# Optimization experiments

Measured on AMD Instinct MI355X. Metric: run time of the kernel, lower is better.

Reference implementation:

```python
import jax, jax.numpy as jnp
import numpy as np

B, N, FIN = 32, 1024, 6
KCHEB = 3
CLASS_NUM = 40


def _pairwise_adj(x):
    # x: [B, N, D] -> exp(-squared_euclidean_dist) adjacency [B, N, N]
    inner = jnp.einsum('bnd,bmd->bnm', x, x)
    sq = jnp.sum(x * x, axis=-1)
    d2 = sq[:, :, None] - 2.0 * inner + sq[:, None, :]
    return jnp.exp(-d2)


def _get_laplacian(adj):
    # normalized Laplacian: I - D^{-1/2} A D^{-1/2}
    deg = jnp.sum(adj, axis=-1)                       # [B, N]
    d_is = 1.0 / jnp.sqrt(deg)                        # [B, N]
    eye = jnp.eye(adj.shape[-1], dtype=adj.dtype)
    return eye - d_is[:, :, None] * adj * d_is[:, None, :]


def _cheb_conv(x, L, W, b):
    # Chebyshev graph conv: sum_k T_k(L) x W_k + b;  W: [K, Fin, Fout]
    x0 = x
    x1 = jnp.einsum('bnm,bmf->bnf', L, x0)
    out = jnp.einsum('bnf,fg->bng', x0, W[0]) + jnp.einsum('bnf,fg->bng', x1, W[1])
    xk_2, xk_1 = x0, x1
    for k in range(2, W.shape[0]):
        xk = 2.0 * jnp.einsum('bnm,bmf->bnf', L, xk_1) - xk_2
        out = out + jnp.einsum('bnf,fg->bng', xk, W[k])
        xk_2, xk_1 = xk_1, xk
    return out + b


def setup_inputs() -> dict:
    key = jax.random.key(0)
    ks = jax.random.split(key, 16)

    def w(k, shape, fan_in):
        return jax.random.normal(k, shape, dtype=jnp.float32) / np.sqrt(fan_in)

    return {
        'x': jax.random.normal(ks[0], (B, N, FIN), dtype=jnp.float32),
        'W1': w(ks[1], (KCHEB, 6, 128), 6 * KCHEB),
        'b1': jnp.zeros((128,), jnp.float32),
        'W2': w(ks[2], (KCHEB, 128, 512), 128 * KCHEB),
        'b2': jnp.zeros((512,), jnp.float32),
        'W3': w(ks[3], (KCHEB, 512, 1024), 512 * KCHEB),
        'b3': jnp.zeros((1024,), jnp.float32),
        'fc1_w': w(ks[4], (1024, 512), 1024),
        'fc1_b': jnp.zeros((512,), jnp.float32),
        'fc2_w': w(ks[5], (512, 128), 512),
        'fc2_b': jnp.zeros((128,), jnp.float32),
        'fc3_w': w(ks[6], (128, CLASS_NUM), 128),
        'fc3_b': jnp.zeros((CLASS_NUM,), jnp.float32),
    }


def reference(x, W1, b1, W2, b2, W3, b3, fc1_w, fc1_b, fc2_w, fc2_b, fc3_w, fc3_b):
    # Laplacians are computed under torch.no_grad in the original
    L = _get_laplacian(_pairwise_adj(x))
    out = jax.nn.relu(_cheb_conv(x, L, W1, b1))        # [B, N, 128]

    L = _get_laplacian(_pairwise_adj(out))
    out = jax.nn.relu(_cheb_conv(out, L, W2, b2))      # [B, N, 512]

    L = _get_laplacian(_pairwise_adj(out))
    out = jax.nn.relu(_cheb_conv(out, L, W3, b3))      # [B, N, 1024]

    out = jnp.max(out, axis=1)                          # global max pool -> [B, 1024]
    out = jax.nn.relu(out @ fc1_w + fc1_b)              # dropout is identity at eval
    out = jax.nn.relu(out @ fc2_w + fc2_b)
    out = out @ fc3_w + fc3_b                           # [B, CLASS_NUM]
    return out
```

## Files before the change

### kernel.cpp

```cpp
#include <hip/hip_runtime.h>
#include <cstddef>


#define NN 1024

typedef unsigned short ushort_t;
typedef __bf16 bf16x8 __attribute__((ext_vector_type(8)));
typedef float f32x4 __attribute__((ext_vector_type(4)));

__device__ inline ushort_t f2bf(float f) {
    unsigned int u = __float_as_uint(f);
    u = (u + 0x7fffu + ((u >> 16) & 1u)) >> 16;
    return (ushort_t)u;
}
__device__ inline float bf2f(ushort_t s) {
    return __uint_as_float(((unsigned int)s) << 16);
}

__device__ __attribute__((always_inline)) inline void gld16(
    const ushort_t* g, ushort_t* l) {
    __builtin_amdgcn_global_load_lds(
        (__attribute__((address_space(1))) void*)(ushort_t*)g,
        (__attribute__((address_space(3))) void*)l, 16, 0, 0);
}

__global__ void zero_kernel(float* __restrict__ p, int n) {
    int i = blockIdx.x * blockDim.x + threadIdx.x;
    if (i < n) p[i] = 0.f;
}

__global__ __launch_bounds__(256) void wconvT_kernel(
    const float* __restrict__ W, ushort_t* __restrict__ Wt, int Fi, int Fo, int Ks) {
    int p = blockIdx.z;
    int k0 = blockIdx.y * 64, g0 = blockIdx.x * 64;
    __shared__ float T[64][65];
    int t = threadIdx.x;
#pragma unroll
    for (int q = 0; q < 16; ++q) {
        int kr = (t >> 6) + 4 * q, gc = t & 63;
        int k = k0 + kr, g = g0 + gc;
        T[kr][gc] = (k < Fi && g < Fo) ? W[((size_t)p * Fi + k) * Fo + g] : 0.f;
    }
    __syncthreads();
#pragma unroll
    for (int q = 0; q < 16; ++q) {
        int gr = (t >> 6) + 4 * q, kc = t & 63;
        int g = g0 + gr, k = k0 + kc;
        if (g < Fo && k < Ks)
            Wt[((size_t)p * Fo + g) * Ks + k] = f2bf(T[kc][gr]);
    }
}

__global__ __launch_bounds__(256) void prep2_kernel(
    const float* __restrict__ X, ushort_t* __restrict__ hi, ushort_t* __restrict__ lo,
    ushort_t* __restrict__ Xt, float* __restrict__ sq, int F, int Fp, int bsh) {
    int L = blockIdx.x;
    int b = L & ((1 << bsh) - 1), n0 = (L >> bsh) * 64;
    int t = threadIdx.x;
    __shared__ float T[64][65];
    __shared__ float red[4][64];
    const float* Xb = X + ((size_t)b * NN + n0) * F;
    float sacc = 0.f;

    for (int f0 = 0; f0 < Fp; f0 += 64) {
        __syncthreads();
#pragma unroll
        for (int p = 0; p < 16; ++p) {
            int nr = (t >> 6) + 4 * p, fc = t & 63;
            int f = f0 + fc;
            T[nr][fc] = (f < F) ? Xb[(size_t)nr * F + f] : 0.f;
        }
        __syncthreads();
#pragma unroll
        for (int p = 0; p < 16; ++p) {
            int nr = (t >> 6) + 4 * p, fc = t & 63;
            int f = f0 + fc;
            if (f < Fp) {
                float x = T[nr][fc];
                ushort_t h = f2bf(x);
                size_t off = ((size_t)b * NN + n0 + nr) * Fp + f;
                hi[off] = h;
                lo[off] = f2bf(x - bf2f(h));
            }
        }
#pragma unroll
        for (int p = 0; p < 16; ++p) {
            int fr = (t >> 6) + 4 * p;
            int f = f0 + fr;
            if (f < F)
                Xt[((size_t)b * Fp + f) * NN + n0 + (t & 63)] = f2bf(T[t & 63][fr]);
        }
        {
            int nl = t & 63, fq = t >> 6;
#pragma unroll
            for (int fc = 0; fc < 16; ++fc) {
                float v = T[nl][fq * 16 + fc];
                sacc += v * v;
            }
        }
    }
    red[t >> 6][t & 63] = sacc;
    __syncthreads();
    if (t < 64)
        sq[(size_t)b * NN + n0 + t] = red[0][t] + red[1][t] + red[2][t] + red[3][t];
}

__global__ __launch_bounds__(256) void adj_kernel(
    const ushort_t* __restrict__ hi, const ushort_t* __restrict__ lo,
    const float* __restrict__ sq, ushort_t* __restrict__ Abf,
    float* __restrict__ deg_part, int Fp, int bsh, int BCv) {
    int t = threadIdx.x;
    int L = blockIdx.x;
    int b = L & ((1 << bsh) - 1);
    int rest = L >> bsh;
    int m0 = (rest & 7) * 128, n0 = (rest >> 3) * 128;
    const ushort_t* Hb = hi + (size_t)b * NN * Fp;
    const ushort_t* Lb = lo + (size_t)b * NN * Fp;
    ushort_t* Ab = Abf + (size_t)b * NN * NN;
    const float* sqb = sq + (size_t)b * NN;

    int lane = t & 63, quad = lane >> 4, l16 = lane & 15, wave = t >> 6;
    int rowoff = (wave >> 1) * 64, coloff = (wave & 1) * 64;

    __shared__ __align__(16) ushort_t smem[40960];

    f32x4 acc[4][4];
#pragma unroll
    for (int i = 0; i < 4; ++i)
#pragma unroll
        for (int j = 0; j < 4; ++j) acc[i][j] = (f32x4){0.f, 0.f, 0.f, 0.f};

    int rr0 = t >> 2, kq = (t & 3) * 8;
    int rr1 = rr0 + 64;
    const ushort_t* pAh0 = Hb + (size_t)(n0 + rr0) * Fp + kq;
    const ushort_t* pAh1 = Hb + (size_t)(n0 + rr1) * Fp + kq;
    const ushort_t* pAl0 = Lb + (size_t)(n0 + rr0) * Fp + kq;
    const ushort_t* pAl1 = Lb + (size_t)(n0 + rr1) * Fp + kq;
    const ushort_t* pBh0 = Hb + (size_t)(m0 + rr0) * Fp + kq;
    const ushort_t* pBh1 = Hb + (size_t)(m0 + rr1) * Fp + kq;
    const ushort_t* pBl0 = Lb + (size_t)(m0 + rr0) * Fp + kq;
    const ushort_t* pBl1 = Lb + (size_t)(m0 + rr1) * Fp + kq;
    int o0 = rr0 * 40 + kq, o1 = rr1 * 40 + kq;

    {
        *(uint4*)&smem[o0]         = *(const uint4*)pAh0;
        *(uint4*)&smem[o1]         = *(const uint4*)pAh1;
        *(uint4*)&smem[5120 + o0]  = *(const uint4*)pAl0;
        *(uint4*)&smem[5120 + o1]  = *(const uint4*)pAl1;
        *(uint4*)&smem[10240 + o0] = *(const uint4*)pBh0;
        *(uint4*)&smem[10240 + o1] = *(const uint4*)pBh1;
        *(uint4*)&smem[15360 + o0] = *(const uint4*)pBl0;
        *(uint4*)&smem[15360 + o1] = *(const uint4*)pBl1;
    }
    __syncthreads();

    int NIT = Fp >> 5;
    for (int it = 0; it < NIT; ++it) {
        int cur = (it & 1) * 20480;
        int nxt = 20480 - cur;
        uint4 rh0, rh1, rl0, rl1, sh0, sh1, sl0, sl1;
        if (it + 1 < NIT) {
            int k = (it + 1) * 32;
            rh0 = *(const uint4*)(pAh0 + k); rh1 = *(const uint4*)(pAh1 + k);
            rl0 = *(const uint4*)(pAl0 + k); rl1 = *(const uint4*)(pAl1 + k);
            sh0 = *(const uint4*)(pBh0 + k); sh1 = *(const uint4*)(pBh1 + k);
            sl0 = *(const uint4*)(pBl0 + k); sl1 = *(const uint4*)(pBl1 + k);
        }
        ushort_t* Ah = smem + cur;
        ushort_t* Al = smem + cur + 5120;
        ushort_t* Bh = smem + cur + 10240;
        ushort_t* Bl = smem + cur + 15360;
        bf16x8 ah[4], al[4], bh[4], bl[4];
#pragma unroll
        for (int i = 0; i < 4; ++i) {
            ah[i] = *(const bf16x8*)&Ah[(rowoff + i * 16 + l16) * 40 + quad * 8];
            al[i] = *(const bf16x8*)&Al[(rowoff + i * 16 + l16) * 40 + quad * 8];
        }
#pragma unroll
        for (int j = 0; j < 4; ++j) {
            bh[j] = *(const bf16x8*)&Bh[(coloff + j * 16 + l16) * 40 + quad * 8];
            bl[j] = *(const bf16x8*)&Bl[(coloff + j * 16 + l16) * 40 + quad * 8];
        }
#pragma unroll
        for (int i = 0; i < 4; ++i)
#pragma unroll
            for (int j = 0; j < 4; ++j) {
                acc[i][j] = __builtin_amdgcn_mfma_f32_16x16x32_bf16(al[i], bh[j], acc[i][j], 0, 0, 0);
                acc[i][j] = __builtin_amdgcn_mfma_f32_16x16x32_bf16(ah[i], bl[j], acc[i][j], 0, 0, 0);
                acc[i][j] = __builtin_amdgcn_mfma_f32_16x16x32_bf16(ah[i], bh[j], acc[i][j], 0, 0, 0);
            }
        if (it + 1 < NIT) {
            *(uint4*)&smem[nxt + o0]         = rh0;
            *(uint4*)&smem[nxt + o1]         = rh1;
            *(uint4*)&smem[nxt + 5120 + o0]  = rl0;
            *(uint4*)&smem[nxt + 5120 + o1]  = rl1;
            *(uint4*)&smem[nxt + 10240 + o0] = sh0;
            *(uint4*)&smem[nxt + 10240 + o1] = sh1;
            *(uint4*)&smem[nxt + 15360 + o0] = sl0;
            *(uint4*)&smem[nxt + 15360 + o1] = sl1;
        }
        __syncthreads();
    }

    float rs[4][4];
#pragma unroll
    for (int i = 0; i < 4; ++i)
#pragma unroll
        for (int r = 0; r < 4; ++r) rs[i][r] = 0.f;

#pragma unroll
    for (int j = 0; j < 4; ++j) {
        int m = m0 + coloff + j * 16 + l16;
        float sm = sqb[m];
#pragma unroll
        for (int i = 0; i < 4; ++i) {
#pragma unroll
            for (int r = 0; r < 4; ++r) {
                int n = n0 + rowoff + i * 16 + quad * 4 + r;
                float v = __expf(2.f * acc[i][j][r] - sqb[n] - sm);
                Ab[(size_t)n * NN + m] = f2bf(v);
                rs[i][r] += v;
            }
        }
    }
    int slot = (rest & 7) * 2 + (wave & 1);
#pragma unroll
    for (int i = 0; i < 4; ++i)
#pragma unroll
        for (int r = 0; r < 4; ++r) {
            float s = rs[i][r];
            s += __shfl_xor(s, 1);
            s += __shfl_xor(s, 2);
            s += __shfl_xor(s, 4);
            s += __shfl_xor(s, 8);
            if (l16 == 0)
                deg_part[((size_t)slot * BCv + b) * NN + n0 + rowoff + i * 16 + quad * 4 + r] = s;
        }
}

__global__ __launch_bounds__(256) void disscale_kernel(
    ushort_t* __restrict__ Xt, const float* __restrict__ deg_part,
    float* __restrict__ dis, int Fp, int bsh, int BCv) {
    int L = blockIdx.x;
    int b = L & ((1 << bsh) - 1), n0 = (L >> bsh) * 64;
    int t = threadIdx.x;
    __shared__ float dloc[64];
    if (t < 64) {
        float s = 0.f;
#pragma unroll
        for (int k = 0; k < 16; ++k) s += deg_part[((size_t)k * BCv + b) * NN + n0 + t];
        float d = rsqrtf(s);
        dloc[t] = d;
        dis[(size_t)b * NN + n0 + t] = d;
    }
    __syncthreads();
    int lane = t & 63, fq = t >> 6;
    float d = dloc[lane];
    ushort_t* Xb = Xt + (size_t)b * Fp * NN + n0 + lane;
    for (int f = fq; f < Fp; f += 4) {
        size_t off = (size_t)f * NN;
        Xb[off] = f2bf(bf2f(Xb[off]) * d);
    }
}

__global__ __launch_bounds__(256) void lx_kernel(
    const ushort_t* __restrict__ Abf, const float* __restrict__ dis,
    const ushort_t* __restrict__ in_t, const ushort_t* __restrict__ x0t,
    ushort_t* __restrict__ out_t, ushort_t* __restrict__ out_b,
    int F, int Fp, int mode, int ft, int bsh) {
    int t = threadIdx.x;
    int L = blockIdx.x;
    int b = L & ((1 << bsh) - 1);
    int rest = L >> bsh;
    int m0 = (rest % ft) * 128;
    int n0 = (rest / ft) * 64;
    const ushort_t* Ain = in_t + (size_t)b * Fp * NN;
    const ushort_t* Ab = Abf + (size_t)b * NN * NN;

    int lane = t & 63, quad = lane >> 4, l16 = lane & 15, wave = t >> 6;
    int rowoff = wave * 32;

    __shared__ __align__(16) ushort_t smem[18432];

    f32x4 acc[2][4];
#pragma unroll
    for (int i = 0; i < 2; ++i)
#pragma unroll
        for (int j = 0; j < 4; ++j) acc[i][j] = (f32x4){0.f, 0.f, 0.f, 0.f};

    int lr = lane >> 2, lk = (lane & 3) * 8;
    int rbase = wave * 32;
    const ushort_t* gA = Ain + (size_t)(m0 + rbase + lr) * NN + lk;
    const ushort_t* gB = Ab + (size_t)(n0 + wave * 16 + lr) * NN + lk;

#define LX_STAGE(BOFF, CI)                                            \
    {                                                                 \
        int k_ = (CI) * 32;                                           \
        ushort_t* As_ = smem + (BOFF);                                \
        gld16(gA + k_, As_ + rbase * 32);                             \
        gld16(gA + (size_t)16 * NN + k_, As_ + rbase * 32 + 512);     \
        gld16(gB + k_, As_ + 4096 + wave * 16 * 32);                  \
    }
#define LX_COMP(BOFF)                                                            \
    {                                                                            \
        ushort_t* As_ = smem + (BOFF);                                           \
        ushort_t* Bs_ = As_ + 4096;                                              \
        bf16x8 af[2], bfv[4];                                                    \
        _Pragma("unroll")                                                        \
        for (int i = 0; i < 2; ++i)                                              \
            af[i] = *(const bf16x8*)&As_[(rowoff + i * 16 + l16) * 32 + quad * 8]; \
        _Pragma("unroll")                                                        \
        for (int j = 0; j < 4; ++j)                                              \
            bfv[j] = *(const bf16x8*)&Bs_[(j * 16 + l16) * 32 + quad * 8];       \
        _Pragma("unroll")                                                        \
        for (int i = 0; i < 2; ++i)                                              \
            _Pragma("unroll")                                                    \
            for (int j = 0; j < 4; ++j)                                          \
                acc[i][j] = __builtin_amdgcn_mfma_f32_16x16x32_bf16(af[i], bfv[j], acc[i][j], 0, 0, 0); \
    }

    LX_STAGE(0, 0);
    LX_STAGE(6144, 1);
    int cur = 0;
    for (int ci = 0; ci < 32; ++ci) {
        if (ci < 31) { asm volatile("s_waitcnt vmcnt(3)" ::: "memory"); }
        else         { asm volatile("s_waitcnt vmcnt(0)" ::: "memory"); }
        __builtin_amdgcn_s_barrier();
        asm volatile("" ::: "memory");
        if (ci + 2 < 32) {
            int noff = cur + 12288; if (noff >= 18432) noff -= 18432;
            LX_STAGE(noff, ci + 2);
        }
        LX_COMP(cur);
        cur += 6144; if (cur >= 18432) cur = 0;
    }
#undef LX_STAGE
#undef LX_COMP
    __syncthreads();

#pragma unroll
    for (int j = 0; j < 4; ++j) {
        int nl = j * 16 + l16;
        int n = n0 + nl;
        float dn = dis[(size_t)b * NN + n];
        float inv = 1.f / dn;
        float dn2 = dn * dn;
#pragma unroll
        for (int i = 0; i < 2; ++i) {
#pragma unroll
            for (int r = 0; r < 4; ++r) {
                int fl = rowoff + i * 16 + quad * 4 + r;
                int f = m0 + fl;
                float o = 0.f;
                if (f < F) {
                    float a = acc[i][j][r];
                    size_t off = (size_t)f * NN + n;
                    float xin = bf2f(Ain[off]);
                    if (mode == 0) {
                        out_t[(size_t)b * Fp * NN + off] = f2bf(xin - dn2 * a);
                        o = inv * xin - dn * a;
                    } else {
                        float x0 = bf2f(x0t[(size_t)b * Fp * NN + off]);
                        o = inv * (2.f * xin - x0) - 2.f * dn * a;
                    }
                }
                smem[nl * 128 + (((fl >> 3) ^ (nl & 7)) << 3) + (fl & 7)] = f2bf(o);
            }
        }
    }
    __syncthreads();
    for (int s2 = t; s2 < 1024; s2 += 256) {
        int nl = s2 >> 4, oct = s2 & 15;
        int fg = m0 + oct * 8;
        if (fg < Fp) {
            uint4 v = *(const uint4*)&smem[nl * 128 + ((oct ^ (nl & 7)) << 3)];
            *(uint4*)(out_b + ((size_t)b * NN + n0 + nl) * Fp + fg) = v;
        }
    }
}

__global__ __launch_bounds__(256) void proj_kernel(
    const ushort_t* __restrict__ X0, const ushort_t* __restrict__ X1,
    const ushort_t* __restrict__ X2, const ushort_t* __restrict__ Wt,
    const float* __restrict__ bias, float* __restrict__ O, float* __restrict__ pool,
    int Fp, int Fo, int b0, int n_g, int bsh) {
    int t = threadIdx.x;
    int L = blockIdx.x;
    int c = L & ((1 << bsh) - 1);
    int rest = L >> bsh;
    int g0 = (rest % n_g) * 128;
    int r0 = (c * 8 + rest / n_g) * 128;
    int lane = t & 63, quad = lane >> 4, l16 = lane & 15, wave = t >> 6;
    int rowoff = (wave >> 1) * 64, coloff = (wave & 1) * 64;

    __shared__ __align__(16) ushort_t smem[24576];

    f32x4 acc[4][4];
#pragma unroll
    for (int i = 0; i < 4; ++i)
#pragma unroll
        for (int j = 0; j < 4; ++j) acc[i][j] = (f32x4){0.f, 0.f, 0.f, 0.f};

    int lr = lane >> 2, lk = (lane & 3) * 8;
    int rbase = wave * 32;
    int nk = Fp >> 5;
    int NIT = 3 * nk;
    size_t FoFp = (size_t)Fo * Fp;
    size_t r16 = (size_t)16 * Fp;

#define PJ_STAGE(BOFF, CI)                                                    \
    {                                                                         \
        int p_ = (CI) / nk;                                                   \
        int k_ = ((CI) - p_ * nk) * 32 + lk;                                  \
        const ushort_t* Xp_ = (p_ == 0) ? X0 : ((p_ == 1) ? X1 : X2);         \
        const ushort_t* ga_ = Xp_ + (size_t)(r0 + rbase + lr) * Fp + k_;      \
        const ushort_t* gb_ = Wt + (size_t)p_ * FoFp +                        \
                              (size_t)(g0 + rbase + lr) * Fp + k_;            \
        ushort_t* As_ = smem + (BOFF);                                        \
        ushort_t* Bs_ = As_ + 4096;                                           \
        gld16(ga_, As_ + rbase * 32);                                         \
        gld16(ga_ + r16, As_ + rbase * 32 + 512);                             \
        gld16(gb_, Bs_ + rbase * 32);                                         \
        gld16(gb_ + r16, Bs_ + rbase * 32 + 512);                             \
    }
#define PJ_COMP(BOFF)                                                            \
    {                                                                            \
        ushort_t* As_ = smem + (BOFF);                                           \
        ushort_t* Bs_ = As_ + 4096;                                              \
        bf16x8 af[4], bfv[4];                                                    \
        _Pragma("unroll")                                                        \
        for (int i = 0; i < 4; ++i)                                              \
            af[i] = *(const bf16x8*)&As_[(rowoff + i * 16 + l16) * 32 + quad * 8];  \
        _Pragma("unroll")                                                        \
        for (int j = 0; j < 4; ++j)                                              \
            bfv[j] = *(const bf16x8*)&Bs_[(coloff + j * 16 + l16) * 32 + quad * 8]; \
        _Pragma("unroll")                                                        \
        for (int i = 0; i < 4; ++i)                                              \
            _Pragma("unroll")                                                    \
            for (int j = 0; j < 4; ++j)                                          \
                acc[i][j] = __builtin_amdgcn_mfma_f32_16x16x32_bf16(af[i], bfv[j], acc[i][j], 0, 0, 0); \
    }

    PJ_STAGE(0, 0);
    PJ_STAGE(8192, 1);
    int cur = 0;
    for (int ci = 0; ci < NIT; ++ci) {
        if (ci < NIT - 1) { asm volatile("s_waitcnt vmcnt(4)" ::: "memory"); }
        else              { asm volatile("s_waitcnt vmcnt(0)" ::: "memory"); }
        __builtin_amdgcn_s_barrier();
        asm volatile("" ::: "memory");
        if (ci + 2 < NIT) {
            int noff = cur + 16384; if (noff >= 24576) noff -= 24576;
            PJ_STAGE(noff, ci + 2);
        }
        PJ_COMP(cur);
        cur += 8192; if (cur >= 24576) cur = 0;
    }
#undef PJ_STAGE
#undef PJ_COMP

    float bias_l[4];
#pragma unroll
    for (int j = 0; j < 4; ++j) bias_l[j] = bias[g0 + coloff + j * 16 + l16];

    if (O) {
#pragma unroll
        for (int i = 0; i < 4; ++i) {
#pragma unroll
            for (int r = 0; r < 4; ++r) {
                int row = r0 + rowoff + i * 16 + quad * 4 + r;
#pragma unroll
                for (int j = 0; j < 4; ++j) {
                    int g = g0 + coloff + j * 16 + l16;
                    O[(size_t)row * Fo + g] = fmaxf(acc[i][j][r] + bias_l[j], 0.f);
                }
            }
        }
    } else {
        float mj[4];
#pragma unroll
        for (int j = 0; j < 4; ++j) {
            float m = 0.f;
#pragma unroll
            for (int i = 0; i < 4; ++i)
#pragma unroll
                for (int r = 0; r < 4; ++r)
                    m = fmaxf(m, acc[i][j][r] + bias_l[j]);
            m = fmaxf(m, 0.f);
            m = fmaxf(m, __shfl_xor(m, 16));
            m = fmaxf(m, __shfl_xor(m, 32));
            mj[j] = m;
        }
        if (quad == 0) {
            int smp = b0 + (r0 >> 10);
#pragma unroll
            for (int j = 0; j < 4; ++j)
                atomicMax((int*)&pool[(size_t)smp * 1024 + g0 + coloff + j * 16 + l16],
                          __float_as_int(mj[j]));
        }
    }
}

__global__ __launch_bounds__(256) void fc_kernel(
    const float* __restrict__ In, const float* __restrict__ W,
    const float* __restrict__ bias, float* __restrict__ out,
    int K, int Nout, int relu) {
    int r = blockIdx.y;
    int c0 = blockIdx.x * 64;
    int t = threadIdx.x;
    int cl = t & 63, ks = t >> 6;
    int c = c0 + cl;
    int kchunk = K >> 2;
    int k0 = ks * kchunk, k1 = k0 + kchunk;
    float s = 0.f;
    if (c < Nout) {
        const float* ip = In + (size_t)r * K;
        const float* wp = W + c;
#pragma unroll 4
        for (int k = k0; k < k1; ++k) s += ip[k] * wp[(size_t)k * Nout];
    }
    __shared__ float red[4][64];
    red[ks][cl] = s;
    __syncthreads();
    if (t < 64 && c0 + t < Nout) {
        float v = red[0][t] + red[1][t] + red[2][t] + red[3][t] + bias[c0 + t];
        if (relu) v = fmaxf(v, 0.f);
        out[(size_t)r * Nout + c0 + t] = v;
    }
}

extern "C" void kernel_launch(void* const* d_in, const int* in_sizes, int n_in,
                              void* d_out, int out_size, void* d_ws, size_t ws_size,
                              hipStream_t stream) {
    const float* x    = (const float*)d_in[0];
    const float* W1   = (const float*)d_in[1];
    const float* b1   = (const float*)d_in[2];
    const float* W2   = (const float*)d_in[3];
    const float* b2   = (const float*)d_in[4];
    const float* W3   = (const float*)d_in[5];
    const float* b3   = (const float*)d_in[6];
    const float* fc1w = (const float*)d_in[7];
    const float* fc1b = (const float*)d_in[8];
    const float* fc2w = (const float*)d_in[9];
    const float* fc2b = (const float*)d_in[10];
    const float* fc3w = (const float*)d_in[11];
    const float* fc3b = (const float*)d_in[12];
    float* out = (float*)d_out;

    auto need = [](size_t BCv) -> size_t {
        size_t us = (size_t)BCv * 1024;
        return 2 * (us * 1024) + 10 * (us * 512) + 2 * 1781760ull +
               4 * (us * 128) + 4 * (us * 512) + 4 * us + 64 * us + 4 * us +
               4 * (32768ull + 16384 + 4096) + 256;
    };
    int BCv = (ws_size >= need(16)) ? 16 : 8;
    int NCH = 32 / BCv;
    int bsh = (BCv == 16) ? 4 : 3;

    size_t usc = (size_t)BCv * 1024;
    size_t Asz = usc * 1024;
    size_t SLv = usc * 512;
    ushort_t* Abf  = (ushort_t*)d_ws;
    ushort_t* X0hi = Abf + Asz;
    ushort_t* X0lo = X0hi + SLv;
    ushort_t* X0t  = X0lo + SLv;
    ushort_t* X1t  = X0t + SLv;
    ushort_t* X1b  = X1t + SLv;
    ushort_t* Wt   = X1b + SLv;
    float* O1   = (float*)(Wt + 1781760);
    float* O2   = O1 + usc * 128;
    float* sq   = O2 + usc * 512;
    float* degp = sq + usc;
    float* dis  = degp + 16 * usc;
    float* pool = dis + usc;
    float* f1   = pool + 32768;
    float* f2   = f1 + 16384;
    ushort_t* X2b = X0lo;

    wconvT_kernel<<<dim3(2, 1, 3), 256, 0, stream>>>(W1, Wt, 6, 128, 32);
    wconvT_kernel<<<dim3(8, 2, 3), 256, 0, stream>>>(W2, Wt + 12288, 128, 512, 128);
    wconvT_kernel<<<dim3(16, 8, 3), 256, 0, stream>>>(W3, Wt + 208896, 512, 1024, 512);
    zero_kernel<<<128, 256, 0, stream>>>(pool, 32768);

    for (int c = 0; c < NCH; ++c) {
        int b0 = c * BCv;
        struct LayerDef {
            const float* X; int F, Fp, Fo;
            const ushort_t* Wtl; const float* bias; float* O;
        };
        LayerDef L[3] = {
            { x + (size_t)b0 * NN * 6, 6,   32,  128,  Wt,          b1, O1 },
            { O1,                      128, 128, 512,  Wt + 12288,  b2, O2 },
            { O2,                      512, 512, 1024, Wt + 208896, b3, nullptr },
        };
        for (int li = 0; li < 3; ++li) {
            LayerDef& Ld = L[li];
            int F = Ld.F, Fp = Ld.Fp;
            int ft = (F + 127) / 128;
            int n_g = Ld.Fo / 128;
            prep2_kernel<<<16 * BCv, 256, 0, stream>>>(Ld.X, X0hi, X0lo, X0t, sq, F, Fp, bsh);
            adj_kernel<<<64 * BCv, 256, 0, stream>>>(X0hi, X0lo, sq, Abf, degp, Fp, bsh, BCv);
            disscale_kernel<<<16 * BCv, 256, 0, stream>>>(X0t, degp, dis, Fp, bsh, BCv);
            lx_kernel<<<ft * 16 * BCv, 256, 0, stream>>>(
                Abf, dis, X0t, nullptr, X1t, X1b, F, Fp, 0, ft, bsh);
            lx_kernel<<<ft * 16 * BCv, 256, 0, stream>>>(
                Abf, dis, X1t, X0t, nullptr, X2b, F, Fp, 1, ft, bsh);
            proj_kernel<<<n_g * 8 * BCv, 256, 0, stream>>>(
                X0hi, X1b, X2b, Ld.Wtl, Ld.bias, Ld.O, pool, Fp, Ld.Fo, b0, n_g, bsh);
        }
    }

    fc_kernel<<<dim3(8, 32), 256, 0, stream>>>(pool, fc1w, fc1b, f1, 1024, 512, 1);
    fc_kernel<<<dim3(2, 32), 256, 0, stream>>>(f1, fc2w, fc2b, f2, 512, 128, 1);
    fc_kernel<<<dim3(1, 32), 256, 0, stream>>>(f2, fc3w, fc3b, out, 128, 40, 0);
}
```

Measured before the change: 958.7 us.

## Load A operand directly to registers and prioritize MFMA waves

In the Lx and projection GEMM kernels, the A operand no longer goes through LDS. Each wave now loads its own A rows straight from global memory into registers, double-buffered across a two-step unrolled loop, and only B is staged in LDS. This cuts LDS traffic and footprint, which may allow more resident blocks. s_setprio is also raised around the MFMA blocks, including in the 3-pass bf16 split kernel. The risks are higher register pressure, duplicate global reads of A by the two waves sharing rows in the projection kernel, and the hand-tuned vmcnt counts now mixing register loads with LDS-direct loads.

Measured after the change: 1.156 ms. 1.21x slower.

```diff
diff --git a/kernel.cpp b/kernel.cpp
--- a/kernel.cpp
+++ b/kernel.cpp
@@ -181,6 +181,7 @@
             bh[j] = *(const bf16x8*)&Bh[(coloff + j * 16 + l16) * 40 + quad * 8];
             bl[j] = *(const bf16x8*)&Bl[(coloff + j * 16 + l16) * 40 + quad * 8];
         }
+        __builtin_amdgcn_s_setprio(1);
 #pragma unroll
         for (int i = 0; i < 4; ++i)
 #pragma unroll
@@ -189,6 +190,7 @@
                 acc[i][j] = __builtin_amdgcn_mfma_f32_16x16x32_bf16(ah[i], bl[j], acc[i][j], 0, 0, 0);
                 acc[i][j] = __builtin_amdgcn_mfma_f32_16x16x32_bf16(ah[i], bh[j], acc[i][j], 0, 0, 0);
             }
+        __builtin_amdgcn_s_setprio(0);
         if (it + 1 < NIT) {
             *(uint4*)&smem[nxt + o0]         = rh0;
             *(uint4*)&smem[nxt + o1]         = rh1;
@@ -280,7 +282,7 @@
     int lane = t & 63, quad = lane >> 4, l16 = lane & 15, wave = t >> 6;
     int rowoff = wave * 32;
 
-    __shared__ __align__(16) ushort_t smem[18432];
+    __shared__ __align__(16) ushort_t smem[8192];
 
     f32x4 acc[2][4];
 #pragma unroll
@@ -289,52 +291,68 @@
         for (int j = 0; j < 4; ++j) acc[i][j] = (f32x4){0.f, 0.f, 0.f, 0.f};
 
     int lr = lane >> 2, lk = (lane & 3) * 8;
-    int rbase = wave * 32;
-    const ushort_t* gA = Ain + (size_t)(m0 + rbase + lr) * NN + lk;
     const ushort_t* gB = Ab + (size_t)(n0 + wave * 16 + lr) * NN + lk;
-
-#define LX_STAGE(BOFF, CI)                                            \
+    const ushort_t* gA = Ain + (size_t)(m0 + rowoff + l16) * NN + quad * 8;
+
+#define LX_BSTAGE(BOFF, CI)                                           \
     {                                                                 \
-        int k_ = (CI) * 32;                                           \
-        ushort_t* As_ = smem + (BOFF);                                \
-        gld16(gA + k_, As_ + rbase * 32);                             \
-        gld16(gA + (size_t)16 * NN + k_, As_ + rbase * 32 + 512);     \
-        gld16(gB + k_, As_ + 4096 + wave * 16 * 32);                  \
-    }
-#define LX_COMP(BOFF)                                                            \
+        gld16(gB + (CI) * 32, smem + (BOFF) + wave * 512);            \
+    }
+#define LX_ALOAD(CI, A0, A1)                                          \
+    {                                                                 \
+        const ushort_t* pa_ = gA + (CI) * 32;                         \
+        A0 = *(const bf16x8*)(pa_);                                   \
+        A1 = *(const bf16x8*)(pa_ + (size_t)16 * NN);                 \
+    }
+#define LX_COMP(BOFF, A0, A1)                                                    \
     {                                                                            \
-        ushort_t* As_ = smem + (BOFF);                                           \
-        ushort_t* Bs_ = As_ + 4096;                                              \
-        bf16x8 af[2], bfv[4];                                                    \
-        _Pragma("unroll")                                                        \
-        for (int i = 0; i < 2; ++i)                                              \
-            af[i] = *(const bf16x8*)&As_[(rowoff + i * 16 + l16) * 32 + quad * 8]; \
+        ushort_t* Bs_ = smem + (BOFF);                                           \
+        bf16x8 bfv[4];                                                           \
         _Pragma("unroll")                                                        \
         for (int j = 0; j < 4; ++j)                                              \
             bfv[j] = *(const bf16x8*)&Bs_[(j * 16 + l16) * 32 + quad * 8];       \
+        __builtin_amdgcn_s_setprio(1);                                           \
         _Pragma("unroll")                                                        \
-        for (int i = 0; i < 2; ++i)                                              \
-            _Pragma("unroll")                                                    \
-            for (int j = 0; j < 4; ++j)                                          \
-                acc[i][j] = __builtin_amdgcn_mfma_f32_16x16x32_bf16(af[i], bfv[j], acc[i][j], 0, 0, 0); \
-    }
-
-    LX_STAGE(0, 0);
-    LX_STAGE(6144, 1);
+        for (int j = 0; j < 4; ++j) {                                            \
+            acc[0][j] = __builtin_amdgcn_mfma_f32_16x16x32_bf16(A0, bfv[j], acc[0][j], 0, 0, 0); \
+            acc[1][j] = __builtin_amdgcn_mfma_f32_16x16x32_bf16(A1, bfv[j], acc[1][j], 0, 0, 0); \
+        }                                                                        \
+        __builtin_amdgcn_s_setprio(0);                                           \
+    }
+
+    bf16x8 ax0, ax1, ay0, ay1;
+    LX_BSTAGE(0, 0);
+    LX_BSTAGE(2048, 1);
+    LX_ALOAD(0, ax0, ax1);
     int cur = 0;
-    for (int ci = 0; ci < 32; ++ci) {
+    for (int pp = 0; pp < 16; ++pp) {
+        int ci = 2 * pp;
         if (ci < 31) { asm volatile("s_waitcnt vmcnt(3)" ::: "memory"); }
-        else         { asm volatile("s_waitcnt vmcnt(0)" ::: "memory"); }
+        else         { asm volatile("s_waitcnt vmcnt(2)" ::: "memory"); }
         __builtin_amdgcn_s_barrier();
         asm volatile("" ::: "memory");
+        LX_ALOAD(ci + 1, ay0, ay1);
         if (ci + 2 < 32) {
-            int noff = cur + 12288; if (noff >= 18432) noff -= 18432;
-            LX_STAGE(noff, ci + 2);
-        }
-        LX_COMP(cur);
-        cur += 6144; if (cur >= 18432) cur = 0;
-    }
-#undef LX_STAGE
+            int noff = cur + 4096; if (noff >= 6144) noff -= 6144;
+            LX_BSTAGE(noff, ci + 2);
+        }
+        LX_COMP(cur, ax0, ax1);
+        cur += 2048; if (cur >= 6144) cur = 0;
+        int cj = ci + 1;
+        if (cj < 31) { asm volatile("s_waitcnt vmcnt(3)" ::: "memory"); }
+        else         { asm volatile("s_waitcnt vmcnt(2)" ::: "memory"); }
+        __builtin_amdgcn_s_barrier();
+        asm volatile("" ::: "memory");
+        if (cj + 1 < 32) LX_ALOAD(cj + 1, ax0, ax1);
+        if (cj + 2 < 32) {
+            int noff = cur + 4096; if (noff >= 6144) noff -= 6144;
+            LX_BSTAGE(noff, cj + 2);
+        }
+        LX_COMP(cur, ay0, ay1);
+        cur += 2048; if (cur >= 6144) cur = 0;
+    }
+#undef LX_BSTAGE
+#undef LX_ALOAD
 #undef LX_COMP
     __syncthreads();
 
@@ -393,7 +411,7 @@
     int lane = t & 63, quad = lane >> 4, l16 = lane & 15, wave = t >> 6;
     int rowoff = (wave >> 1) * 64, coloff = (wave & 1) * 64;
 
-    __shared__ __align__(16) ushort_t smem[24576];
+    __shared__ __align__(16) ushort_t smem[12288];
 
     f32x4 acc[4][4];
 #pragma unroll
@@ -408,55 +426,85 @@
     size_t FoFp = (size_t)Fo * Fp;
     size_t r16 = (size_t)16 * Fp;
 
-#define PJ_STAGE(BOFF, CI)                                                    \
+#define PJ_BSTAGE(BOFF, CI)                                                   \
     {                                                                         \
         int p_ = (CI) / nk;                                                   \
         int k_ = ((CI) - p_ * nk) * 32 + lk;                                  \
-        const ushort_t* Xp_ = (p_ == 0) ? X0 : ((p_ == 1) ? X1 : X2);         \
-        const ushort_t* ga_ = Xp_ + (size_t)(r0 + rbase + lr) * Fp + k_;      \
         const ushort_t* gb_ = Wt + (size_t)p_ * FoFp +                        \
                               (size_t)(g0 + rbase + lr) * Fp + k_;            \
-        ushort_t* As_ = smem + (BOFF);                                        \
-        ushort_t* Bs_ = As_ + 4096;                                           \
-        gld16(ga_, As_ + rbase * 32);                                         \
-        gld16(ga_ + r16, As_ + rbase * 32 + 512);                             \
-        gld16(gb_, Bs_ + rbase * 32);                                         \
-        gld16(gb_ + r16, Bs_ + rbase * 32 + 512);                             \
-    }
-#define PJ_COMP(BOFF)                                                            \
+        ushort_t* Bs_ = smem + (BOFF) + rbase * 32;                           \
+        gld16(gb_, Bs_);                                                      \
+        gld16(gb_ + r16, Bs_ + 512);                                          \
+    }
+#define PJ_ALOAD(CI, A0, A1, A2, A3)                                          \
+    {                                                                         \
+        int p_ = (CI) / nk;                                                   \
+        int k_ = ((CI) - p_ * nk) * 32;                                       \
+        const ushort_t* Xp_ = (p_ == 0) ? X0 : ((p_ == 1) ? X1 : X2);         \
+        const ushort_t* pa_ = Xp_ + (size_t)(r0 + rowoff + l16) * Fp + k_ + quad * 8; \
+        A0 = *(const bf16x8*)(pa_);                                           \
+        A1 = *(const bf16x8*)(pa_ + (size_t)16 * Fp);                         \
+        A2 = *(const bf16x8*)(pa_ + (size_t)32 * Fp);                         \
+        A3 = *(const bf16x8*)(pa_ + (size_t)48 * Fp);                         \
+    }
+#define PJ_COMP(BOFF, A0, A1, A2, A3)                                            \
     {                                                                            \
-        ushort_t* As_ = smem + (BOFF);                                           \
-        ushort_t* Bs_ = As_ + 4096;                                              \
-        bf16x8 af[4], bfv[4];                                                    \
-        _Pragma("unroll")                                                        \
-        for (int i = 0; i < 4; ++i)                                              \
-            af[i] = *(const bf16x8*)&As_[(rowoff + i * 16 + l16) * 32 + quad * 8];  \
+        ushort_t* Bs_ = smem + (BOFF);                                           \
+        bf16x8 bfv[4];                                                           \
         _Pragma("unroll")                                                        \
         for (int j = 0; j < 4; ++j)                                              \
             bfv[j] = *(const bf16x8*)&Bs_[(coloff + j * 16 + l16) * 32 + quad * 8]; \
+        __builtin_amdgcn_s_setprio(1);                                           \
         _Pragma("unroll")                                                        \
-        for (int i = 0; i < 4; ++i)                                              \
-            _Pragma("unroll")                                                    \
-            for (int j = 0; j < 4; ++j)                                          \
-                acc[i][j] = __builtin_amdgcn_mfma_f32_16x16x32_bf16(af[i], bfv[j], acc[i][j], 0, 0, 0); \
-    }
-
-    PJ_STAGE(0, 0);
-    PJ_STAGE(8192, 1);
+        for (int j = 0; j < 4; ++j) {                                            \
+            acc[0][j] = __builtin_amdgcn_mfma_f32_16x16x32_bf16(A0, bfv[j], acc[0][j], 0, 0, 0); \
+            acc[1][j] = __builtin_amdgcn_mfma_f32_16x16x32_bf16(A1, bfv[j], acc[1][j], 0, 0, 0); \
+            acc[2][j] = __builtin_amdgcn_mfma_f32_16x16x32_bf16(A2, bfv[j], acc[2][j], 0, 0, 0); \
+            acc[3][j] = __builtin_amdgcn_mfma_f32_16x16x32_bf16(A3, bfv[j], acc[3][j], 0, 0, 0); \
+        }                                                                        \
+        __builtin_amdgcn_s_setprio(0);                                           \
+    }
+
+    bf16x8 x0_, x1_, x2_, x3_, y0_, y1_, y2_, y3_;
+    PJ_BSTAGE(0, 0);
+    PJ_BSTAGE(4096, 1);
+    PJ_ALOAD(0, x0_, x1_, x2_, x3_);
     int cur = 0;
-    for (int ci = 0; ci < NIT; ++ci) {
-        if (ci < NIT - 1) { asm volatile("s_waitcnt vmcnt(4)" ::: "memory"); }
-        else              { asm volatile("s_waitcnt vmcnt(0)" ::: "memory"); }
+    int pairs = NIT >> 1;
+    for (int pp = 0; pp < pairs; ++pp) {
+        int ci = 2 * pp;
+        if (ci < NIT - 1) { asm volatile("s_waitcnt vmcnt(6)" ::: "memory"); }
+        else              { asm volatile("s_waitcnt vmcnt(4)" ::: "memory"); }
         __builtin_amdgcn_s_barrier();
         asm volatile("" ::: "memory");
+        PJ_ALOAD(ci + 1, y0_, y1_, y2_, y3_);
         if (ci + 2 < NIT) {
-            int noff = cur + 16384; if (noff >= 24576) noff -= 24576;
-            PJ_STAGE(noff, ci + 2);
-        }
-        PJ_COMP(cur);
-        cur += 8192; if (cur >= 24576) cur = 0;
-    }
-#undef PJ_STAGE
+            int noff = cur + 8192; if (noff >= 12288) noff -= 12288;
+            PJ_BSTAGE(noff, ci + 2);
+        }
+        PJ_COMP(cur, x0_, x1_, x2_, x3_);
+        cur += 4096; if (cur >= 12288) cur = 0;
+        int cj = ci + 1;
+        if (cj < NIT - 1) { asm volatile("s_waitcnt vmcnt(6)" ::: "memory"); }
+        else              { asm volatile("s_waitcnt vmcnt(4)" ::: "memory"); }
+        __builtin_amdgcn_s_barrier();
+        asm volatile("" ::: "memory");
+        if (cj + 1 < NIT) PJ_ALOAD(cj + 1, x0_, x1_, x2_, x3_);
+        if (cj + 2 < NIT) {
+            int noff = cur + 8192; if (noff >= 12288) noff -= 12288;
+            PJ_BSTAGE(noff, cj + 2);
+        }
+        PJ_COMP(cur, y0_, y1_, y2_, y3_);
+        cur += 4096; if (cur >= 12288) cur = 0;
+    }
+    if (NIT & 1) {
+        asm volatile("s_waitcnt vmcnt(4)" ::: "memory");
+        __builtin_amdgcn_s_barrier();
+        asm volatile("" ::: "memory");
+        PJ_COMP(cur, x0_, x1_, x2_, x3_);
+    }
+#undef PJ_BSTAGE
+#undef PJ_ALOAD
 #undef PJ_COMP
 
     float bias_l[4];
```
